# Kernel optimization log

Hardware: AMD Instinct MI355X
Metric: run time of the kernel (lower is better)

Reference implementation:

```python
import jax, jax.numpy as jnp
import numpy as np

EPS = 1e-5
HEADS = 4
DIMK = 16
DIMU = 4
R = 23


def _bn_eval(x, g, b):
    # BatchNorm2d in eval mode with running_mean=0, running_var=1
    return x * (g / np.sqrt(1.0 + EPS))[None, :, None, None] + b[None, :, None, None]


def _conv1x1(x, w):
    # w: (O, C) from a Conv2d(C, O, 1) weight
    return jnp.einsum('bchw,oc->bohw', x, w)


def _lambda_layer(x, wq, wk, wv, qg, qb, vg, vb, pw, pb):
    B, C, H, W = x.shape
    n = H * W
    V = wv.shape[0] // DIMU  # dim_out // heads
    q = _bn_eval(_conv1x1(x, wq), qg, qb).reshape(B, HEADS, DIMK, n)
    k = jax.nn.softmax(_conv1x1(x, wk).reshape(B, DIMU, DIMK, n), axis=-1)
    v = _bn_eval(_conv1x1(x, wv), vg, vb).reshape(B, DIMU, V, n)
    # content lambda: (B, k, v)
    lam_c = jnp.einsum('bukn,buvn->bkv', k, v)
    y_c = jnp.einsum('bhkn,bkv->bhvn', q, lam_c)
    # position lambdas: Conv3d(u, k, (1, R, R)) == 2D conv over (H, W) with v folded into batch
    v5 = v.reshape(B, DIMU, V, H, W).transpose(0, 2, 1, 3, 4).reshape(B * V, DIMU, H, W)
    p = R // 2
    lp = jax.lax.conv_general_dilated(v5, pw, (1, 1), [(p, p), (p, p)],
                                      dimension_numbers=('NCHW', 'OIHW', 'NCHW'))
    lp = lp + pb[None, :, None, None]
    lam_p = lp.reshape(B, V, DIMK, H, W).transpose(0, 2, 1, 3, 4).reshape(B, DIMK, V, n)
    y_p = jnp.einsum('bhkn,bkvn->bhvn', q, lam_p)
    return (y_c + y_p).reshape(B, HEADS * V, H, W)


def _group_norm(x, g, b, groups=8):
    B, C, H, W = x.shape
    xr = x.reshape(B, groups, C // groups, H, W)
    m = xr.mean(axis=(2, 3, 4), keepdims=True)
    var = xr.var(axis=(2, 3, 4), keepdims=True)
    xn = ((xr - m) / jnp.sqrt(var + EPS)).reshape(B, C, H, W)
    return xn * g[None, :, None, None] + b[None, :, None, None]


def setup_inputs() -> dict:
    key = jax.random.key(0)
    B, C, H, W = 4, 64, 192, 192
    V = C // HEADS
    d = {'x': jax.random.normal(jax.random.fold_in(key, 0), (B, C, H, W), jnp.float32)}
    i = 1
    for l in (1, 2, 3):
        for nm, shape, kind in [
            ('wq', (HEADS * DIMK, C), 'w'), ('wk', (DIMU * DIMK, C), 'w'), ('wv', (DIMU * V, C), 'w'),
            ('qg', (HEADS * DIMK,), 'ones'), ('qb', (HEADS * DIMK,), 'zeros'),
            ('vg', (DIMU * V,), 'ones'), ('vb', (DIMU * V,), 'zeros'),
            ('pw', (DIMK, DIMU, R, R), 'w'), ('pb', (DIMK,), 'zeros')]:
            if kind == 'w':
                d['l%d_%s' % (l, nm)] = jax.random.normal(jax.random.fold_in(key, i), shape, jnp.float32) * 0.05
            elif kind == 'ones':
                d['l%d_%s' % (l, nm)] = jnp.ones(shape, jnp.float32)
            else:
                d['l%d_%s' % (l, nm)] = jnp.zeros(shape, jnp.float32)
            i += 1
    d['gn1_g'] = jnp.ones((C,), jnp.float32); d['gn1_b'] = jnp.zeros((C,), jnp.float32)
    d['gn3_g'] = jnp.ones((C,), jnp.float32); d['gn3_b'] = jnp.zeros((C,), jnp.float32)
    d['cw'] = jax.random.normal(jax.random.fold_in(key, 99), (C, C), jnp.float32) * 0.01
    d['cb'] = jnp.zeros((C,), jnp.float32)
    return d


def reference(x,
              l1_wq, l1_wk, l1_wv, l1_qg, l1_qb, l1_vg, l1_vb, l1_pw, l1_pb,
              l2_wq, l2_wk, l2_wv, l2_qg, l2_qb, l2_vg, l2_vb, l2_pw, l2_pb,
              l3_wq, l3_wk, l3_wv, l3_qg, l3_qb, l3_vg, l3_vb, l3_pw, l3_pb,
              gn1_g, gn1_b, gn3_g, gn3_b, cw, cb):
    out = _lambda_layer(x, l1_wq, l1_wk, l1_wv, l1_qg, l1_qb, l1_vg, l1_vb, l1_pw, l1_pb)
    out = _group_norm(out, gn1_g, gn1_b)
    out = _lambda_layer(out, l2_wq, l2_wk, l2_wv, l2_qg, l2_qb, l2_vg, l2_vb, l2_pw, l2_pb)
    out = _group_norm(out, gn1_g, gn1_b)  # original code reuses gn1 here (gn2 unused)
    out = _lambda_layer(out, l3_wq, l3_wk, l3_wv, l3_qg, l3_qb, l3_vg, l3_vb, l3_pw, l3_pb)
    out = _group_norm(out, gn3_g, gn3_b)
    out = _conv1x1(out, cw) + cb[None, :, None, None]
    return out * 0.2 + x
```

## Files before the change

kernel.cpp:

```cpp
#include <hip/hip_runtime.h>

typedef unsigned short USH;
typedef __attribute__((ext_vector_type(8))) short bf16x8;
typedef __attribute__((ext_vector_type(4))) float f32x4;

#define MFMA16(a,b,c) __builtin_amdgcn_mfma_f32_16x16x32_bf16((a),(b),(c),0,0,0)

#define BB 4
#define HH 192
#define NN 36864
#define NTOT 147456
#define CSTR 120
#define NCH 192

__device__ __forceinline__ float bf2f(USH h) {
    union { unsigned int u; float f; } v; v.u = ((unsigned int)h) << 16; return v.f;
}
__device__ __forceinline__ USH f2bf(float f) {
    union { float f; unsigned int u; } v; v.f = f;
    unsigned int u = v.u;
    return (USH)((u + 0x7FFFu + ((u >> 16) & 1u)) >> 16);
}

struct PrepArgs {
    const float* wq[3]; const float* wk[3]; const float* wv[3];
    const float* qg[3]; const float* qb[3]; const float* vg[3]; const float* vb[3];
    const float* pw[3]; const float* cw;
};
__global__ void prep_all_k(PrepArgs pa, USH* __restrict__ apc, USH* __restrict__ apq,
                           float* __restrict__ biasq, USH* __restrict__ apf) {
    int bid = blockIdx.x, tid = threadIdx.x;
    if (bid < 552) {
        int L = bid / 184, cb = bid - L * 184;
        int t = cb * 256 + tid;
        if (t < 736 * 64) {
            const float* pw = pa.pw[L];
            USH* ap = apc + (size_t)L * 376832;
            int lane = t & 63, cg = t >> 6;
            int dy = cg % 23; int ru = cg / 23; int u = ru & 3; int r = ru >> 2;
            int kk = lane & 15, q8 = (lane >> 4) * 8;
            for (int j = 0; j < 8; ++j) {
                int k = q8 + j, dx = k - r - 1;
                USH w = 0;
                if (dx >= 0 && dx < 23) w = f2bf(pw[((kk * 4 + u) * 23 + dy) * 23 + dx]);
                ap[t * 8 + j] = w;
            }
        }
    } else if (bid < 570) {
        int idx = bid - 552; int L = idx / 6; int qblk = idx - L * 6;
        int t = qblk * 256 + tid;
        USH* apl = apq + (size_t)L * 12288;
        float* bl = biasq + L * 192;
        if (t < 1536) {
            int lane = t & 63, chunk = t >> 6;
            int mt = chunk >> 1, kc = chunk & 1;
            int o = mt * 16 + (lane & 15);
            int c0 = kc * 32 + (lane >> 4) * 8;
            float scale; const float* wrow;
            if (o < 64)       { scale = pa.qg[L][o]       * rsqrtf(1.0f + 1e-5f); wrow = pa.wq[L] + o * 64; }
            else if (o < 128) { scale = 1.0f;                                     wrow = pa.wk[L] + (o - 64) * 64; }
            else              { scale = pa.vg[L][o - 128] * rsqrtf(1.0f + 1e-5f); wrow = pa.wv[L] + (o - 128) * 64; }
            for (int j = 0; j < 8; ++j) apl[t * 8 + j] = f2bf(wrow[c0 + j] * scale);
        }
        if (t < 192) {
            float bvv;
            if (t < 64) bvv = pa.qb[L][t]; else if (t < 128) bvv = 0.0f; else bvv = pa.vb[L][t - 128];
            bl[t] = bvv;
        }
    } else {
        int t = (bid - 570) * 256 + tid;
        if (t < 512) {
            int lane = t & 63, chunk = t >> 6;
            int mt = chunk >> 1, kc = chunk & 1;
            int o = mt * 16 + (lane & 15);
            int c0 = kc * 32 + (lane >> 4) * 8;
            for (int j = 0; j < 8; ++j) apf[t * 8 + j] = f2bf(pa.cw[o * 64 + c0 + j]);
        }
    }
}

__global__ __launch_bounds__(256) void x_qkv_k(
    const float* __restrict__ xin, const bf16x8* __restrict__ apre, const float* __restrict__ bias,
    USH* __restrict__ qT, USH* __restrict__ kbuf, USH* __restrict__ vbuf) {
    __shared__ float tf[64][65];
    const int bid = blockIdx.x; const int b = bid / 576; const int nt = bid - b * 576; const int n0 = nt * 64;
    const int tid = threadIdx.x, lane = tid & 63, wq = tid >> 6;
    const int nl = lane & 15, quad = lane >> 4;
    bf16x8 afr[24];
    #pragma unroll
    for (int i = 0; i < 24; ++i) afr[i] = apre[i * 64 + lane];
    #pragma unroll
    for (int p = 0; p < 16; ++p) {
        int idx = p * 256 + tid; int c = idx >> 6, nn = idx & 63;
        tf[nn][c] = xin[((size_t)b * 64 + c) * NN + n0 + nn];
    }
    __syncthreads();
    bf16x8 b0, b1;
    #pragma unroll
    for (int j = 0; j < 8; ++j) {
        b0[j] = (short)f2bf(tf[wq * 16 + nl][quad * 8 + j]);
        b1[j] = (short)f2bf(tf[wq * 16 + nl][32 + quad * 8 + j]);
    }
    const int n = n0 + wq * 16 + nl;
    #pragma unroll
    for (int mt = 0; mt < 12; ++mt) {
        f32x4 acc = {0.f, 0.f, 0.f, 0.f};
        acc = MFMA16(afr[mt * 2 + 0], b0, acc);
        acc = MFMA16(afr[mt * 2 + 1], b1, acc);
        int o0 = mt * 16 + quad * 4;
        float4 bs = *(const float4*)(bias + o0);
        float v0 = acc[0] + bs.x, v1 = acc[1] + bs.y, v2 = acc[2] + bs.z, v3 = acc[3] + bs.w;
        if (mt < 4) {
            ushort4 pk; pk.x = f2bf(v0); pk.y = f2bf(v1); pk.z = f2bf(v2); pk.w = f2bf(v3);
            *(ushort4*)(qT + ((size_t)b * NN + n) * 64 + o0) = pk;
        } else if (mt < 8) {
            int ko = o0 - 64;
            kbuf[((size_t)b * 64 + ko    ) * NN + n] = f2bf(v0);
            kbuf[((size_t)b * 64 + ko + 1) * NN + n] = f2bf(v1);
            kbuf[((size_t)b * 64 + ko + 2) * NN + n] = f2bf(v2);
            kbuf[((size_t)b * 64 + ko + 3) * NN + n] = f2bf(v3);
        } else {
            int u = mt - 8, vv0 = quad * 4;
            vbuf[(((size_t)b * 16 + vv0    ) * 4 + u) * NN + n] = f2bf(v0);
            vbuf[(((size_t)b * 16 + vv0 + 1) * 4 + u) * NN + n] = f2bf(v1);
            vbuf[(((size_t)b * 16 + vv0 + 2) * 4 + u) * NN + n] = f2bf(v2);
            vbuf[(((size_t)b * 16 + vv0 + 3) * 4 + u) * NN + n] = f2bf(v3);
        }
    }
}

__global__ __launch_bounds__(1024) void softstat_k(const USH* __restrict__ kbuf,
                                                   float* __restrict__ kstat) {
    __shared__ USH row_s[NN];
    __shared__ float red[64];
    const USH* p = kbuf + (size_t)blockIdx.x * NN;
    int tid = threadIdx.x, lane = tid & 63, w = tid >> 6;
    float m = -1e30f;
    for (int i = tid * 4; i < NN; i += 4096) {
        ushort4 t4 = *(const ushort4*)(p + i);
        *(ushort4*)(row_s + i) = t4;
        m = fmaxf(m, fmaxf(fmaxf(bf2f(t4.x), bf2f(t4.y)), fmaxf(bf2f(t4.z), bf2f(t4.w))));
    }
    for (int off = 32; off; off >>= 1) m = fmaxf(m, __shfl_down(m, off));
    if (lane == 0) red[w] = m;
    __syncthreads();
    if (tid == 0) { float mm = red[0]; for (int i = 1; i < 16; ++i) mm = fmaxf(mm, red[i]); red[16] = mm; }
    __syncthreads();
    float M = red[16];
    float s = 0.f;
    for (int i = tid * 4; i < NN; i += 4096) {
        ushort4 t4 = *(const ushort4*)(row_s + i);
        s += __expf(bf2f(t4.x) - M) + __expf(bf2f(t4.y) - M)
           + __expf(bf2f(t4.z) - M) + __expf(bf2f(t4.w) - M);
    }
    for (int off = 32; off; off >>= 1) s += __shfl_down(s, off);
    if (lane == 0) red[32 + w] = s;
    __syncthreads();
    if (tid == 0) {
        float ss = 0.f;
        for (int i = 0; i < 16; ++i) ss += red[32 + i];
        kstat[blockIdx.x * 2]     = M;
        kstat[blockIdx.x * 2 + 1] = 1.0f / ss;
    }
}

__global__ __launch_bounds__(64) void lamc_stage1_k(
    const USH* __restrict__ kbuf, const USH* __restrict__ vbuf,
    const float* __restrict__ kstat, float* __restrict__ part) {
    int bid = blockIdx.x;
    int cidx = bid >> 4; int rem = bid & 15; int b = rem >> 2; int u = rem & 3;
    int lane = threadIdx.x; int nl = lane & 15, quad = lane >> 4;
    int krow = b * 64 + u * 16 + nl;
    float M = kstat[krow * 2], inv = kstat[krow * 2 + 1];
    const USH* kp = kbuf + (size_t)krow * NN + cidx * 192 + quad * 8;
    const USH* vp = vbuf + (((size_t)b * 16 + nl) * 4 + u) * NN + cidx * 192 + quad * 8;
    f32x4 acc = {0.f, 0.f, 0.f, 0.f};
    #pragma unroll
    for (int s = 0; s < 6; ++s) {
        bf16x8 kr = *(const bf16x8*)(kp + s * 32);
        bf16x8 va = *(const bf16x8*)(vp + s * 32);
        bf16x8 ka;
        #pragma unroll
        for (int j = 0; j < 8; ++j)
            ka[j] = (short)f2bf(__expf(bf2f((USH)kr[j]) - M) * inv);
        acc = MFMA16(ka, va, acc);
    }
    float* pout = part + ((size_t)(cidx * 4 + b) * 4 + u) * 256;
    #pragma unroll
    for (int rg = 0; rg < 4; ++rg)
        pout[nl * 16 + quad * 4 + rg] = acc[rg];
}

__global__ __launch_bounds__(256, 3) void conv_pos_fused_k(
    const USH* __restrict__ vbuf, const bf16x8* __restrict__ apre,
    const USH* __restrict__ qT, const float* __restrict__ lcp,
    const float* __restrict__ pb, USH* __restrict__ yb, float* __restrict__ gnp2) {
    __shared__ __align__(16) USH in_s[4 * 54 * CSTR];
    __shared__ float lc_red[16][16];
    __shared__ float lc_s[16];
    __shared__ float gn_s[16], gn_q[16];
    const int xh = blockIdx.x, yt = blockIdx.y, img = blockIdx.z;
    const int b = img >> 4, vvch = img & 15;
    const int tid = threadIdx.x;
    {
        int kk = tid & 15, slice = tid >> 4;
        float s = 0.f;
        for (int p = slice * 48; p < slice * 48 + 48; ++p) {
            int cidx = p >> 2, u = p & 3;
            s += lcp[((size_t)(cidx * 4 + b) * 4 + u) * 256 + vvch * 16 + kk];
        }
        lc_red[slice][kk] = s;
    }
    {
        const USH* vb = vbuf + (size_t)img * 4 * NN;
        const int y0 = yt * 32 - 11, x0 = xh * 96 - 12;
        for (int i4 = tid; i4 < 6480; i4 += 256) {
            int u = i4 / 1620;
            int rem = i4 - u * 1620;
            int rr = rem / 30;
            int cc = (rem - rr * 30) * 4;
            int gy = y0 + rr, gx = x0 + cc;
            ushort4 val = {0, 0, 0, 0};
            if (gy >= 0 && gy < HH && gx >= 0 && gx <= HH - 4)
                val = *(const ushort4*)(vb + u * NN + gy * HH + gx);
            *(ushort4*)(in_s + (u * 54 + rr) * CSTR + cc) = val;
        }
    }
    __syncthreads();
    if (tid < 16) {
        float s = 0.f;
        #pragma unroll
        for (int sl = 0; sl < 16; ++sl) s += lc_red[sl][tid];
        lc_s[tid] = s + pb[tid];
    }
    __syncthreads();

    const int lane = tid & 63, wv = tid >> 6;
    const int wy = wv >> 1, wx = wv & 1;
    const int nl = lane & 15, quad = lane >> 4;
    const USH* sbase = in_s + (wy * 16 + nl) * CSTR + wx * 48 + quad * 8;
    const int ybase = yt * 32 + wy * 16 + nl;
    float lcr0 = lc_s[quad * 4], lcr1 = lc_s[quad * 4 + 1],
          lcr2 = lc_s[quad * 4 + 2], lcr3 = lc_s[quad * 4 + 3];
    const USH* qbase = qT + ((size_t)b * NN + ybase * HH) * 64 + quad * 4;
    USH* ybbase = yb + ((size_t)b * 64 + quad * 16 + vvch) * NN + ybase * HH;
    float SG = 0.f, QG = 0.f;

#define CONV_EPILOGUE(ACC, RVAL)                                                            \
    {                                                                                       \
        _Pragma("unroll")                                                                   \
        for (int xi = 0; xi < 6; ++xi) {                                                    \
            int x = xh * 96 + wx * 48 + (RVAL) + 8 * xi;                                    \
            float l0 = ACC[xi][0] + lcr0, l1 = ACC[xi][1] + lcr1;                           \
            float l2 = ACC[xi][2] + lcr2, l3 = ACC[xi][3] + lcr3;                           \
            const USH* qp = qbase + (size_t)x * 64;                                         \
            float s0, s1, s2, s3;                                                           \
            {                                                                               \
                ushort4 q4 = *(const ushort4*)(qp);                                         \
                s0 = bf2f(q4.x) * l0 + bf2f(q4.y) * l1 + bf2f(q4.z) * l2 + bf2f(q4.w) * l3; \
            }                                                                               \
            {                                                                               \
                ushort4 q4 = *(const ushort4*)(qp + 16);                                    \
                s1 = bf2f(q4.x) * l0 + bf2f(q4.y) * l1 + bf2f(q4.z) * l2 + bf2f(q4.w) * l3; \
            }                                                                               \
            {                                                                               \
                ushort4 q4 = *(const ushort4*)(qp + 32);                                    \
                s2 = bf2f(q4.x) * l0 + bf2f(q4.y) * l1 + bf2f(q4.z) * l2 + bf2f(q4.w) * l3; \
            }                                                                               \
            {                                                                               \
                ushort4 q4 = *(const ushort4*)(qp + 48);                                    \
                s3 = bf2f(q4.x) * l0 + bf2f(q4.y) * l1 + bf2f(q4.z) * l2 + bf2f(q4.w) * l3; \
            }                                                                               \
            s0 += __shfl_xor(s0, 16); s0 += __shfl_xor(s0, 32);                             \
            s1 += __shfl_xor(s1, 16); s1 += __shfl_xor(s1, 32);                             \
            s2 += __shfl_xor(s2, 16); s2 += __shfl_xor(s2, 32);                             \
            s3 += __shfl_xor(s3, 16); s3 += __shfl_xor(s3, 32);                             \
            float sel = (quad == 0) ? s0 : (quad == 1) ? s1 : (quad == 2) ? s2 : s3;        \
            USH wo = f2bf(sel);                                                             \
            ybbase[x] = wo;                                                                 \
            float wf = bf2f(wo);                                                            \
            SG += wf; QG += wf * wf;                                                        \
        }                                                                                   \
    }

#define CONV_PASS3(R0)                                                                      \
    {                                                                                       \
        f32x4 acc0[6] = {}; f32x4 acc1[6] = {}; f32x4 acc2[6] = {};                         \
        for (int u = 0; u < 4; ++u) {                                                       \
            const bf16x8* ap0 = apre + ((size_t)((R0) * 4 + u) * 23) * 64 + lane;           \
            const bf16x8* ap1 = ap0 + 4 * 23 * 64;                                          \
            const bf16x8* ap2 = ap0 + 2 * 4 * 23 * 64;                                      \
            const USH* srow = sbase + u * (54 * CSTR);                                      \
            _Pragma("unroll 2")                                                             \
            for (int dy = 0; dy < 23; ++dy) {                                               \
                bf16x8 a0 = *ap0, a1 = *ap1, a2 = *ap2;                                     \
                _Pragma("unroll")                                                           \
                for (int xi = 0; xi < 6; ++xi) {                                            \
                    bf16x8 bfr = *(const bf16x8*)(srow + 8 * xi);                           \
                    acc0[xi] = MFMA16(a0, bfr, acc0[xi]);                                   \
                    acc1[xi] = MFMA16(a1, bfr, acc1[xi]);                                   \
                    acc2[xi] = MFMA16(a2, bfr, acc2[xi]);                                   \
                }                                                                           \
                ap0 += 64; ap1 += 64; ap2 += 64; srow += CSTR;                               \
            }                                                                               \
        }                                                                                   \
        CONV_EPILOGUE(acc0, (R0))                                                           \
        CONV_EPILOGUE(acc1, (R0) + 1)                                                       \
        CONV_EPILOGUE(acc2, (R0) + 2)                                                       \
    }

    CONV_PASS3(0)
    CONV_PASS3(3)
    {
        f32x4 acc0[6] = {}; f32x4 acc1[6] = {};
        for (int u = 0; u < 4; ++u) {
            const bf16x8* ap0 = apre + ((size_t)(6 * 4 + u) * 23) * 64 + lane;
            const bf16x8* ap1 = ap0 + 4 * 23 * 64;
            const USH* srow = sbase + u * (54 * CSTR);
            #pragma unroll 2
            for (int dy = 0; dy < 23; ++dy) {
                bf16x8 a0 = *ap0, a1 = *ap1;
                #pragma unroll
                for (int xi = 0; xi < 6; ++xi) {
                    bf16x8 bfr = *(const bf16x8*)(srow + 8 * xi);
                    acc0[xi] = MFMA16(a0, bfr, acc0[xi]);
                    acc1[xi] = MFMA16(a1, bfr, acc1[xi]);
                }
                ap0 += 64; ap1 += 64; srow += CSTR;
            }
        }
        CONV_EPILOGUE(acc0, 6)
        CONV_EPILOGUE(acc1, 7)
    }
#undef CONV_PASS3
#undef CONV_EPILOGUE

    SG += __shfl_xor(SG, 1); SG += __shfl_xor(SG, 2); SG += __shfl_xor(SG, 4); SG += __shfl_xor(SG, 8);
    QG += __shfl_xor(QG, 1); QG += __shfl_xor(QG, 2); QG += __shfl_xor(QG, 4); QG += __shfl_xor(QG, 8);
    if (nl == 0) { gn_s[wv * 4 + quad] = SG; gn_q[wv * 4 + quad] = QG; }
    __syncthreads();
    if (tid < 4) {
        float s = gn_s[tid] + gn_s[4 + tid] + gn_s[8 + tid] + gn_s[12 + tid];
        float q = gn_q[tid] + gn_q[4 + tid] + gn_q[8 + tid] + gn_q[12 + tid];
        int lin = img * 12 + yt * 2 + xh;
        gnp2[lin * 8 + tid * 2]     = s;
        gnp2[lin * 8 + tid * 2 + 1] = q;
    }
}

__global__ __launch_bounds__(256) void gn_qkv_k(
    const USH* __restrict__ yb, const float* __restrict__ gnp2,
    const float* __restrict__ gg, const float* __restrict__ gb,
    const bf16x8* __restrict__ apre, const float* __restrict__ bias,
    USH* __restrict__ qT, USH* __restrict__ kbuf, USH* __restrict__ vbuf) {
    __shared__ float tf[64][65];
    __shared__ float sc[64], sb[64];
    __shared__ float grs[64], grq[64], st_s[16];
    const int bid = blockIdx.x; const int b = bid / 576; const int nt = bid - b * 576; const int n0 = nt * 64;
    const int tid = threadIdx.x, lane = tid & 63, wq = tid >> 6;
    const int nl = lane & 15, quad = lane >> 4;
    bf16x8 afr[24];
    #pragma unroll
    for (int i = 0; i < 24; ++i) afr[i] = apre[i * 64 + lane];
    if (tid < 64) {
        int g = tid >> 3, vv = tid & 7;
        int qg = g >> 1, v0 = (g & 1) * 8;
        float s = 0.f, q = 0.f;
        #pragma unroll
        for (int tile = 0; tile < 12; ++tile) {
            const float* p = gnp2 + ((size_t)((b * 16 + v0 + vv) * 12 + tile)) * 8 + qg * 2;
            s += p[0]; q += p[1];
        }
        grs[tid] = s; grq[tid] = q;
    }
    __syncthreads();
    if (tid < 8) {
        float s = 0.f, q = 0.f;
        #pragma unroll
        for (int vv = 0; vv < 8; ++vv) { s += grs[tid * 8 + vv]; q += grq[tid * 8 + vv]; }
        float mean = s / 294912.0f;
        float var = q / 294912.0f - mean * mean;
        st_s[tid * 2] = mean;
        st_s[tid * 2 + 1] = rsqrtf(fmaxf(var, 0.0f) + 1e-5f);
    }
    __syncthreads();
    if (tid < 64) {
        int g = tid >> 3;
        float mean = st_s[g * 2], rstd = st_s[g * 2 + 1];
        float ga = gg[tid];
        sc[tid] = rstd * ga;
        sb[tid] = gb[tid] - mean * rstd * ga;
    }
    __syncthreads();
    #pragma unroll
    for (int p = 0; p < 4; ++p) {
        int c = p * 16 + (tid >> 4), nn = (tid & 15) * 4;
        ushort4 y4 = *(const ushort4*)(yb + ((size_t)b * 64 + c) * NN + n0 + nn);
        float scc = sc[c], sbc = sb[c];
        tf[nn][c]     = bf2f(y4.x) * scc + sbc;
        tf[nn + 1][c] = bf2f(y4.y) * scc + sbc;
        tf[nn + 2][c] = bf2f(y4.z) * scc + sbc;
        tf[nn + 3][c] = bf2f(y4.w) * scc + sbc;
    }
    __syncthreads();
    bf16x8 b0, b1;
    #pragma unroll
    for (int j = 0; j < 8; ++j) {
        b0[j] = (short)f2bf(tf[wq * 16 + nl][quad * 8 + j]);
        b1[j] = (short)f2bf(tf[wq * 16 + nl][32 + quad * 8 + j]);
    }
    const int n = n0 + wq * 16 + nl;
    #pragma unroll
    for (int mt = 0; mt < 12; ++mt) {
        f32x4 acc = {0.f, 0.f, 0.f, 0.f};
        acc = MFMA16(afr[mt * 2 + 0], b0, acc);
        acc = MFMA16(afr[mt * 2 + 1], b1, acc);
        int o0 = mt * 16 + quad * 4;
        float4 bs = *(const float4*)(bias + o0);
        float v0 = acc[0] + bs.x, v1 = acc[1] + bs.y, v2 = acc[2] + bs.z, v3 = acc[3] + bs.w;
        if (mt < 4) {
            ushort4 pk; pk.x = f2bf(v0); pk.y = f2bf(v1); pk.z = f2bf(v2); pk.w = f2bf(v3);
            *(ushort4*)(qT + ((size_t)b * NN + n) * 64 + o0) = pk;
        } else if (mt < 8) {
            int ko = o0 - 64;
            kbuf[((size_t)b * 64 + ko    ) * NN + n] = f2bf(v0);
            kbuf[((size_t)b * 64 + ko + 1) * NN + n] = f2bf(v1);
            kbuf[((size_t)b * 64 + ko + 2) * NN + n] = f2bf(v2);
            kbuf[((size_t)b * 64 + ko + 3) * NN + n] = f2bf(v3);
        } else {
            int u = mt - 8, vv0 = quad * 4;
            vbuf[(((size_t)b * 16 + vv0    ) * 4 + u) * NN + n] = f2bf(v0);
            vbuf[(((size_t)b * 16 + vv0 + 1) * 4 + u) * NN + n] = f2bf(v1);
            vbuf[(((size_t)b * 16 + vv0 + 2) * 4 + u) * NN + n] = f2bf(v2);
            vbuf[(((size_t)b * 16 + vv0 + 3) * 4 + u) * NN + n] = f2bf(v3);
        }
    }
}

__global__ __launch_bounds__(256) void gn_final_k(
    const USH* __restrict__ yb, const float* __restrict__ gnp2,
    const float* __restrict__ gg, const float* __restrict__ gb,
    const bf16x8* __restrict__ apre, const float* __restrict__ cb,
    const float* __restrict__ xin, float* __restrict__ out) {
    __shared__ float tf[64][65];
    __shared__ float sc[64], sb[64];
    __shared__ float grs[64], grq[64], st_s[16];
    const int bid = blockIdx.x; const int b = bid / 576; const int nt = bid - b * 576; const int n0 = nt * 64;
    const int tid = threadIdx.x, lane = tid & 63, wq = tid >> 6;
    const int nl = lane & 15, quad = lane >> 4;
    bf16x8 afr[8];
    #pragma unroll
    for (int i = 0; i < 8; ++i) afr[i] = apre[i * 64 + lane];
    if (tid < 64) {
        int g = tid >> 3, vv = tid & 7;
        int qg = g >> 1, v0 = (g & 1) * 8;
        float s = 0.f, q = 0.f;
        #pragma unroll
        for (int tile = 0; tile < 12; ++tile) {
            const float* p = gnp2 + ((size_t)((b * 16 + v0 + vv) * 12 + tile)) * 8 + qg * 2;
            s += p[0]; q += p[1];
        }
        grs[tid] = s; grq[tid] = q;
    }
    __syncthreads();
    if (tid < 8) {
        float s = 0.f, q = 0.f;
        #pragma unroll
        for (int vv = 0; vv < 8; ++vv) { s += grs[tid * 8 + vv]; q += grq[tid * 8 + vv]; }
        float mean = s / 294912.0f;
        float var = q / 294912.0f - mean * mean;
        st_s[tid * 2] = mean;
        st_s[tid * 2 + 1] = rsqrtf(fmaxf(var, 0.0f) + 1e-5f);
    }
    __syncthreads();
    if (tid < 64) {
        int g = tid >> 3;
        float mean = st_s[g * 2], rstd = st_s[g * 2 + 1];
        float ga = gg[tid];
        sc[tid] = rstd * ga;
        sb[tid] = gb[tid] - mean * rstd * ga;
    }
    __syncthreads();
    #pragma unroll
    for (int p = 0; p < 4; ++p) {
        int c = p * 16 + (tid >> 4), nn = (tid & 15) * 4;
        ushort4 y4 = *(const ushort4*)(yb + ((size_t)b * 64 + c) * NN + n0 + nn);
        float scc = sc[c], sbc = sb[c];
        tf[nn][c]     = bf2f(y4.x) * scc + sbc;
        tf[nn + 1][c] = bf2f(y4.y) * scc + sbc;
        tf[nn + 2][c] = bf2f(y4.z) * scc + sbc;
        tf[nn + 3][c] = bf2f(y4.w) * scc + sbc;
    }
    __syncthreads();
    bf16x8 b0, b1;
    #pragma unroll
    for (int j = 0; j < 8; ++j) {
        b0[j] = (short)f2bf(tf[wq * 16 + nl][quad * 8 + j]);
        b1[j] = (short)f2bf(tf[wq * 16 + nl][32 + quad * 8 + j]);
    }
    const int n = n0 + wq * 16 + nl;
    #pragma unroll
    for (int mt = 0; mt < 4; ++mt) {
        f32x4 acc = {0.f, 0.f, 0.f, 0.f};
        acc = MFMA16(afr[mt * 2 + 0], b0, acc);
        acc = MFMA16(afr[mt * 2 + 1], b1, acc);
        int o0 = mt * 16 + quad * 4;
        float4 cb4 = *(const float4*)(cb + o0);
        float cbv[4] = { cb4.x, cb4.y, cb4.z, cb4.w };
        #pragma unroll
        for (int rg = 0; rg < 4; ++rg) {
            int o = o0 + rg;
            float xv = xin[((size_t)b * 64 + o) * NN + n];
            out[((size_t)b * 64 + o) * NN + n] = (acc[rg] + cbv[rg]) * 0.2f + xv;
        }
    }
}

extern "C" void kernel_launch(void* const* d_in, const int* in_sizes, int n_in,
                              void* d_out, int out_size, void* d_ws, size_t ws_size,
                              hipStream_t stream) {
    (void)in_sizes; (void)n_in; (void)out_size; (void)ws_size;
    const float* x = (const float*)d_in[0];
    char* ws = (char*)d_ws;

    const size_t SZP = (size_t)NTOT * 64 * 2;
    USH*   P0 = (USH*)(ws);
    USH*   P1 = (USH*)(ws + SZP);
    USH*   P2 = (USH*)(ws + 2 * SZP);
    USH*   P3 = (USH*)(ws + 3 * SZP);
    char*  tail  = ws + 4 * SZP;
    USH*   apc   = (USH*)(tail);            tail += 753664 * 3;
    USH*   apq   = (USH*)(tail);            tail += 24576 * 3;
    float* biasq = (float*)(tail);          tail += 768 * 3;
    USH*   apf   = (USH*)(tail);            tail += 8192;
    float* lcp   = (float*)(tail);          tail += 3145728;
    float* gnp2  = (float*)(tail);          tail += 24576;
    float* kst   = (float*)(tail);

    PrepArgs pa;
    for (int L = 0; L < 3; ++L) {
        int base = 1 + L * 9;
        pa.wq[L] = (const float*)d_in[base + 0];
        pa.wk[L] = (const float*)d_in[base + 1];
        pa.wv[L] = (const float*)d_in[base + 2];
        pa.qg[L] = (const float*)d_in[base + 3];
        pa.qb[L] = (const float*)d_in[base + 4];
        pa.vg[L] = (const float*)d_in[base + 5];
        pa.vb[L] = (const float*)d_in[base + 6];
        pa.pw[L] = (const float*)d_in[base + 7];
    }
    pa.cw = (const float*)d_in[32];

    prep_all_k<<<572, 256, 0, stream>>>(pa, apc, apq, biasq, apf);

    x_qkv_k<<<2304, 256, 0, stream>>>(x, (const bf16x8*)apq, biasq, P1, P2, P3);

    for (int L = 0; L < 3; ++L) {
        const float* pb = (const float*)d_in[1 + L * 9 + 8];
        USH* kv = (L == 1) ? P0 : P2;

        softstat_k<<<256, 1024, 0, stream>>>(kv, kst);
        lamc_stage1_k<<<NCH * 16, 64, 0, stream>>>(kv, P3, kst, lcp);
        dim3 cg(2, 6, 64);
        conv_pos_fused_k<<<cg, 256, 0, stream>>>(P3, (const bf16x8*)apc + (size_t)L * 47104,
                                                 P1, lcp, pb, kv, gnp2);
        if (L < 2) {
            const float* gg = (const float*)d_in[28];
            const float* gb = (const float*)d_in[29];
            USH* knext = (L == 0) ? P0 : P2;
            gn_qkv_k<<<2304, 256, 0, stream>>>(kv, gnp2, gg, gb,
                                               (const bf16x8*)apq + (size_t)(L + 1) * 1536,
                                               biasq + (L + 1) * 192, P1, knext, P3);
        } else {
            const float* gg = (const float*)d_in[30];
            const float* gb = (const float*)d_in[31];
            gn_final_k<<<2304, 256, 0, stream>>>(kv, gnp2, gg, gb, (const bf16x8*)apf,
                                                 (const float*)d_in[33], x, (float*)d_out);
        }
    }
}
```

Measured before the change: 909.3 us.

## Halve conv tile height and split output-row work across waves for occupancy

```diff
diff --git a/kernel.cpp b/kernel.cpp
--- a/kernel.cpp
+++ b/kernel.cpp
@@ -11,6 +11,7 @@
 #define NN 36864
 #define NTOT 147456
 #define CSTR 120
+#define CROWS 38
 #define NCH 192
 
 __device__ __forceinline__ float bf2f(USH h) {
@@ -191,11 +192,11 @@
         pout[nl * 16 + quad * 4 + rg] = acc[rg];
 }
 
-__global__ __launch_bounds__(256, 3) void conv_pos_fused_k(
+__global__ __launch_bounds__(256, 4) void conv_pos_fused_k(
     const USH* __restrict__ vbuf, const bf16x8* __restrict__ apre,
     const USH* __restrict__ qT, const float* __restrict__ lcp,
     const float* __restrict__ pb, USH* __restrict__ yb, float* __restrict__ gnp2) {
-    __shared__ __align__(16) USH in_s[4 * 54 * CSTR];
+    __shared__ __align__(16) USH in_s[4 * CROWS * CSTR];
     __shared__ float lc_red[16][16];
     __shared__ float lc_s[16];
     __shared__ float gn_s[16], gn_q[16];
@@ -213,17 +214,17 @@
     }
     {
         const USH* vb = vbuf + (size_t)img * 4 * NN;
-        const int y0 = yt * 32 - 11, x0 = xh * 96 - 12;
-        for (int i4 = tid; i4 < 6480; i4 += 256) {
-            int u = i4 / 1620;
-            int rem = i4 - u * 1620;
+        const int y0 = yt * 16 - 11, x0 = xh * 96 - 12;
+        for (int i4 = tid; i4 < 4 * CROWS * 30; i4 += 256) {
+            int u = i4 / (CROWS * 30);
+            int rem = i4 - u * (CROWS * 30);
             int rr = rem / 30;
             int cc = (rem - rr * 30) * 4;
             int gy = y0 + rr, gx = x0 + cc;
             ushort4 val = {0, 0, 0, 0};
             if (gy >= 0 && gy < HH && gx >= 0 && gx <= HH - 4)
                 val = *(const ushort4*)(vb + u * NN + gy * HH + gx);
-            *(ushort4*)(in_s + (u * 54 + rr) * CSTR + cc) = val;
+            *(ushort4*)(in_s + (u * CROWS + rr) * CSTR + cc) = val;
         }
     }
     __syncthreads();
@@ -236,10 +237,10 @@
     __syncthreads();
 
     const int lane = tid & 63, wv = tid >> 6;
-    const int wy = wv >> 1, wx = wv & 1;
+    const int wx = wv & 1, rh = wv >> 1;
     const int nl = lane & 15, quad = lane >> 4;
-    const USH* sbase = in_s + (wy * 16 + nl) * CSTR + wx * 48 + quad * 8;
-    const int ybase = yt * 32 + wy * 16 + nl;
+    const USH* sbase = in_s + nl * CSTR + wx * 48 + quad * 8;
+    const int ybase = yt * 16 + nl;
     float lcr0 = lc_s[quad * 4], lcr1 = lc_s[quad * 4 + 1],
           lcr2 = lc_s[quad * 4 + 2], lcr3 = lc_s[quad * 4 + 3];
     const USH* qbase = qT + ((size_t)b * NN + ybase * HH) * 64 + quad * 4;
@@ -283,56 +284,33 @@
         }                                                                                   \
     }
 
-#define CONV_PASS3(R0)                                                                      \
+#define CONV_PASS2(R0)                                                                      \
     {                                                                                       \
-        f32x4 acc0[6] = {}; f32x4 acc1[6] = {}; f32x4 acc2[6] = {};                         \
+        f32x4 acc0[6] = {}; f32x4 acc1[6] = {};                                             \
         for (int u = 0; u < 4; ++u) {                                                       \
             const bf16x8* ap0 = apre + ((size_t)((R0) * 4 + u) * 23) * 64 + lane;           \
             const bf16x8* ap1 = ap0 + 4 * 23 * 64;                                          \
-            const bf16x8* ap2 = ap0 + 2 * 4 * 23 * 64;                                      \
-            const USH* srow = sbase + u * (54 * CSTR);                                      \
+            const USH* srow = sbase + u * (CROWS * CSTR);                                   \
             _Pragma("unroll 2")                                                             \
             for (int dy = 0; dy < 23; ++dy) {                                               \
-                bf16x8 a0 = *ap0, a1 = *ap1, a2 = *ap2;                                     \
+                bf16x8 a0 = *ap0, a1 = *ap1;                                                \
                 _Pragma("unroll")                                                           \
                 for (int xi = 0; xi < 6; ++xi) {                                            \
                     bf16x8 bfr = *(const bf16x8*)(srow + 8 * xi);                           \
                     acc0[xi] = MFMA16(a0, bfr, acc0[xi]);                                   \
                     acc1[xi] = MFMA16(a1, bfr, acc1[xi]);                                   \
-                    acc2[xi] = MFMA16(a2, bfr, acc2[xi]);                                   \
                 }                                                                           \
-                ap0 += 64; ap1 += 64; ap2 += 64; srow += CSTR;                               \
+                ap0 += 64; ap1 += 64; srow += CSTR;                                          \
             }                                                                               \
         }                                                                                   \
         CONV_EPILOGUE(acc0, (R0))                                                           \
         CONV_EPILOGUE(acc1, (R0) + 1)                                                       \
-        CONV_EPILOGUE(acc2, (R0) + 2)                                                       \
-    }
-
-    CONV_PASS3(0)
-    CONV_PASS3(3)
-    {
-        f32x4 acc0[6] = {}; f32x4 acc1[6] = {};
-        for (int u = 0; u < 4; ++u) {
-            const bf16x8* ap0 = apre + ((size_t)(6 * 4 + u) * 23) * 64 + lane;
-            const bf16x8* ap1 = ap0 + 4 * 23 * 64;
-            const USH* srow = sbase + u * (54 * CSTR);
-            #pragma unroll 2
-            for (int dy = 0; dy < 23; ++dy) {
-                bf16x8 a0 = *ap0, a1 = *ap1;
-                #pragma unroll
-                for (int xi = 0; xi < 6; ++xi) {
-                    bf16x8 bfr = *(const bf16x8*)(srow + 8 * xi);
-                    acc0[xi] = MFMA16(a0, bfr, acc0[xi]);
-                    acc1[xi] = MFMA16(a1, bfr, acc1[xi]);
-                }
-                ap0 += 64; ap1 += 64; srow += CSTR;
-            }
-        }
-        CONV_EPILOGUE(acc0, 6)
-        CONV_EPILOGUE(acc1, 7)
-    }
-#undef CONV_PASS3
+    }
+
+    const int rbase = rh * 4;
+    CONV_PASS2(rbase)
+    CONV_PASS2(rbase + 2)
+#undef CONV_PASS2
 #undef CONV_EPILOGUE
 
     SG += __shfl_xor(SG, 1); SG += __shfl_xor(SG, 2); SG += __shfl_xor(SG, 4); SG += __shfl_xor(SG, 8);
@@ -342,7 +320,7 @@
     if (tid < 4) {
         float s = gn_s[tid] + gn_s[4 + tid] + gn_s[8 + tid] + gn_s[12 + tid];
         float q = gn_q[tid] + gn_q[4 + tid] + gn_q[8 + tid] + gn_q[12 + tid];
-        int lin = img * 12 + yt * 2 + xh;
+        int lin = img * 24 + yt * 2 + xh;
         gnp2[lin * 8 + tid * 2]     = s;
         gnp2[lin * 8 + tid * 2 + 1] = q;
     }
@@ -367,8 +345,8 @@
         int qg = g >> 1, v0 = (g & 1) * 8;
         float s = 0.f, q = 0.f;
         #pragma unroll
-        for (int tile = 0; tile < 12; ++tile) {
-            const float* p = gnp2 + ((size_t)((b * 16 + v0 + vv) * 12 + tile)) * 8 + qg * 2;
+        for (int tile = 0; tile < 24; ++tile) {
+            const float* p = gnp2 + ((size_t)((b * 16 + v0 + vv) * 24 + tile)) * 8 + qg * 2;
             s += p[0]; q += p[1];
         }
         grs[tid] = s; grq[tid] = q;
@@ -456,8 +434,8 @@
         int qg = g >> 1, v0 = (g & 1) * 8;
         float s = 0.f, q = 0.f;
         #pragma unroll
-        for (int tile = 0; tile < 12; ++tile) {
-            const float* p = gnp2 + ((size_t)((b * 16 + v0 + vv) * 12 + tile)) * 8 + qg * 2;
+        for (int tile = 0; tile < 24; ++tile) {
+            const float* p = gnp2 + ((size_t)((b * 16 + v0 + vv) * 24 + tile)) * 8 + qg * 2;
             s += p[0]; q += p[1];
         }
         grs[tid] = s; grq[tid] = q;
@@ -534,7 +512,7 @@
     float* biasq = (float*)(tail);          tail += 768 * 3;
     USH*   apf   = (USH*)(tail);            tail += 8192;
     float* lcp   = (float*)(tail);          tail += 3145728;
-    float* gnp2  = (float*)(tail);          tail += 24576;
+    float* gnp2  = (float*)(tail);          tail += 49152;
     float* kst   = (float*)(tail);
 
     PrepArgs pa;
@@ -561,7 +539,7 @@
 
         softstat_k<<<256, 1024, 0, stream>>>(kv, kst);
         lamc_stage1_k<<<NCH * 16, 64, 0, stream>>>(kv, P3, kst, lcp);
-        dim3 cg(2, 6, 64);
+        dim3 cg(2, 12, 64);
         conv_pos_fused_k<<<cg, 256, 0, stream>>>(P3, (const bf16x8*)apc + (size_t)L * 47104,
                                                  P1, lcp, pb, kv, gnp2);
         if (L < 2) {
```

After: 941.0 us. 1.03x slower.
